# Kernel optimization log

Hardware: AMD Instinct MI355X
Metric: run time of the kernel (lower is better)

Reference implementation:

```python
import jax, jax.numpy as jnp
import numpy as np


def setup_inputs() -> dict:
    key = jax.random.key(0)
    B, Tt, Ts, C = 8, 128, 128, 512
    x = jax.random.normal(key, (B, Tt, Ts, C), dtype=jnp.float32)
    return {"x": x}


def reference(x) -> jnp.ndarray:
    # Original: xpool[:, t, j, :] = max over x[:, t, :j+1, :] along Ts.
    # This is exactly a running (prefix) max along the Ts axis (axis=2);
    # the outer loop over t is independent per row.
    xpool = jax.lax.cummax(x, axis=2)  # [B, Tt, Ts, C]
    return xpool
```

## Files before the change

### kernel.cpp

```cpp
#include <hip/hip_runtime.h>


__global__ __launch_bounds__(256) void cummax_ts_kernel(
    const float4* __restrict__ x, float4* __restrict__ out) {
    constexpr int TS = 128;
    constexpr int CV = 128;

    const int gid = blockIdx.x * blockDim.x + threadIdx.x;
    const int row = gid >> 7;
    const int cv  = gid & (CV - 1);

    const size_t base = (size_t)row * TS * CV + cv;
    const float4* __restrict__ p = x + base;
    float4* __restrict__ q = out + base;

    float4 m = p[0];
    q[0] = m;
#pragma unroll 4
    for (int s = 1; s < TS; ++s) {
        float4 v = p[(size_t)s * CV];
        m.x = fmaxf(m.x, v.x);
        m.y = fmaxf(m.y, v.y);
        m.z = fmaxf(m.z, v.z);
        m.w = fmaxf(m.w, v.w);
        q[(size_t)s * CV] = m;
    }
}

extern "C" void kernel_launch(void* const* d_in, const int* in_sizes, int n_in,
                              void* d_out, int out_size, void* d_ws, size_t ws_size,
                              hipStream_t stream) {
    const float4* x = (const float4*)d_in[0];
    float4* out = (float4*)d_out;

    constexpr int ROWS = 8 * 128;
    constexpr int CV = 128;
    constexpr int BLOCK = 256;
    const int total = ROWS * CV;
    cummax_ts_kernel<<<total / BLOCK, BLOCK, 0, stream>>>(x, out);
}
```

Baseline: 435.0 us.

## Split Ts scan into chunks with shared-memory carry combine

Each row's prefix max along Ts is split into four 32-step chunks handled by separate thread groups. Each group loads its whole chunk into registers up front, scans it locally, and then applies the carry from earlier chunks read out of shared memory. This adds threads and in-flight loads, aiming to remove the latency-bound serial load chain. In exchange it needs high register use and a block barrier.

```diff
diff --git a/kernel.cpp b/kernel.cpp
--- a/kernel.cpp
+++ b/kernel.cpp
@@ -1,41 +1,68 @@
 #include <hip/hip_runtime.h>
 
 
-__global__ __launch_bounds__(256) void cummax_ts_kernel(
+constexpr int TS = 128;
+constexpr int CV = 128;
+constexpr int CHUNK = 32;
+constexpr int NCHUNK = TS / CHUNK;
+constexpr int CVB = 64;
+
+__global__ __launch_bounds__(256, 3) void cummax_scan(
     const float4* __restrict__ x, float4* __restrict__ out) {
-    constexpr int TS = 128;
-    constexpr int CV = 128;
+  __shared__ float4 totals[NCHUNK][CVB];
 
-    const int gid = blockIdx.x * blockDim.x + threadIdx.x;
-    const int row = gid >> 7;
-    const int cv  = gid & (CV - 1);
+  const int tid   = threadIdx.x;
+  const int chunk = tid >> 6;
+  const int cvl   = tid & 63;
+  const int row   = blockIdx.x >> 1;
+  const int cv    = ((blockIdx.x & 1) << 6) | cvl;
 
-    const size_t base = (size_t)row * TS * CV + cv;
-    const float4* __restrict__ p = x + base;
-    float4* __restrict__ q = out + base;
+  const size_t base = ((size_t)row * TS + (size_t)chunk * CHUNK) * CV + cv;
+  const float4* __restrict__ p = x + base;
+  float4*       __restrict__ q = out + base;
 
-    float4 m = p[0];
-    q[0] = m;
-#pragma unroll 4
-    for (int s = 1; s < TS; ++s) {
-        float4 v = p[(size_t)s * CV];
-        m.x = fmaxf(m.x, v.x);
-        m.y = fmaxf(m.y, v.y);
-        m.z = fmaxf(m.z, v.z);
-        m.w = fmaxf(m.w, v.w);
-        q[(size_t)s * CV] = m;
-    }
+  float4 v[CHUNK];
+#pragma unroll
+  for (int i = 0; i < CHUNK; ++i) v[i] = p[(size_t)i * CV];
+
+#pragma unroll
+  for (int i = 1; i < CHUNK; ++i) {
+    v[i].x = fmaxf(v[i].x, v[i - 1].x);
+    v[i].y = fmaxf(v[i].y, v[i - 1].y);
+    v[i].z = fmaxf(v[i].z, v[i - 1].z);
+    v[i].w = fmaxf(v[i].w, v[i - 1].w);
+  }
+
+  totals[chunk][cvl] = v[CHUNK - 1];
+  __syncthreads();
+
+  const float ninf = -__builtin_inff();
+  float4 carry = make_float4(ninf, ninf, ninf, ninf);
+  for (int c = 0; c < chunk; ++c) {
+    float4 t = totals[c][cvl];
+    carry.x = fmaxf(carry.x, t.x);
+    carry.y = fmaxf(carry.y, t.y);
+    carry.z = fmaxf(carry.z, t.z);
+    carry.w = fmaxf(carry.w, t.w);
+  }
+
+#pragma unroll
+  for (int i = 0; i < CHUNK; ++i) {
+    float4 o;
+    o.x = fmaxf(carry.x, v[i].x);
+    o.y = fmaxf(carry.y, v[i].y);
+    o.z = fmaxf(carry.z, v[i].z);
+    o.w = fmaxf(carry.w, v[i].w);
+    q[(size_t)i * CV] = o;
+  }
 }
 
 extern "C" void kernel_launch(void* const* d_in, const int* in_sizes, int n_in,
                               void* d_out, int out_size, void* d_ws, size_t ws_size,
                               hipStream_t stream) {
-    const float4* x = (const float4*)d_in[0];
-    float4* out = (float4*)d_out;
+  const float4* x = (const float4*)d_in[0];
+  float4* out = (float4*)d_out;
 
-    constexpr int ROWS = 8 * 128;
-    constexpr int CV = 128;
-    constexpr int BLOCK = 256;
-    const int total = ROWS * CV;
-    cummax_ts_kernel<<<total / BLOCK, BLOCK, 0, stream>>>(x, out);
+  constexpr int ROWS = 8 * 128;
+  cummax_scan<<<ROWS * 2, 256, 0, stream>>>(x, out);
 }
```

After: 430.9 us. Within noise of the previous version (-0.9%).
